# Performance work log

Measured on AMD Instinct MI355X. Metric: run time of the kernel, lower is better.

The kernel has to match this reference:

```python
import jax, jax.numpy as jnp
import numpy as np

DEPTH = 4
SCALE = 1.0


def _exp_levels(v, depth):
    # Tensor-algebra exponential of a linear segment with increment v: level k = v^{(x)k} / k!
    # v: (B, C); returns tuple of (B, C^k) for k=1..depth
    B = v.shape[0]
    levels = [v]
    for k in range(2, depth + 1):
        levels.append((levels[-1][:, :, None] * v[:, None, :]).reshape(B, -1) / k)
    return tuple(levels)


def _chen_step(levels, v, depth):
    # Chen's identity: S_new = S (x) exp(v), flattened per level.
    e = _exp_levels(v, depth)
    B = v.shape[0]
    new = []
    for k in range(1, depth + 1):
        acc = levels[k - 1] + e[k - 1]
        for i in range(1, k):
            acc = acc + (levels[i - 1][:, :, None] * e[k - i - 1][:, None, :]).reshape(B, -1)
        new.append(acc)
    return tuple(new)


def signature(path, depth):
    # path: (B, T, C) -> concatenated signature levels (B, C + C^2 + ... + C^depth)
    dx = path[:, 1:] - path[:, :-1]          # (B, T-1, C)
    init = _exp_levels(dx[:, 0], depth)      # signature of first segment
    rest = jnp.moveaxis(dx[:, 1:], 0, 1)     # (T-2, B, C)

    def step(lv, v):
        return _chen_step(lv, v, depth), None

    final, _ = jax.lax.scan(step, init, rest)
    return jnp.concatenate(final, axis=-1)


def setup_inputs() -> dict:
    key = jax.random.key(0)
    k1, k2, k3 = jax.random.split(key, 3)
    N, B, T, C = 4096, 1024, 256, 10
    original = jax.random.normal(k1, (N, T, C), dtype=jnp.float32) * 0.1
    generated = jax.random.normal(k2, (B, T, C), dtype=jnp.float32) * 0.1
    sample_idx = jax.random.permutation(k3, N)[:B].astype(jnp.int64)  # sample without replacement
    return {"original": original, "generated": generated, "sample_idx": sample_idx}


def reference(original, generated, sample_idx):
    sig_orig = signature(original, DEPTH)                  # (N, D)
    selected = sig_orig[sample_idx]                        # (B, D)
    sig_gen = signature(generated, DEPTH)                  # (B, D)
    diff = jnp.mean(selected, axis=0) - jnp.mean(sig_gen, axis=0)
    return jnp.linalg.norm(diff) * SCALE
```

## Files before the change

kernel.cpp:

```cpp
#include <hip/hip_runtime.h>

#define T_LEN 256
#define C_DIM 10
#define NSTEP 255
#define BSZ   1024
#define NBLK  2048
#define D1 10
#define D2 100
#define D3 1000
#define DTOT 11110
#define PATH_ELEMS (T_LEN * C_DIM)
#define DX_ELEMS (NSTEP * C_DIM)
#define DXROW 12

__global__ __launch_bounds__(128, 2) void sig_accum_kernel(
    const float* __restrict__ original,
    const float* __restrict__ generated,
    const int* __restrict__ sample_idx,
    float* __restrict__ ws, int nrep, int store_mode)
{
    const int tid = threadIdx.x;
    const int b   = blockIdx.x;

    __shared__ float s_dx[NSTEP * DXROW];

    const float* path;
    float sign;
    if (b < BSZ) { path = original + (size_t)sample_idx[b] * PATH_ELEMS; sign = 1.0f; }
    else         { path = generated + (size_t)(b - BSZ) * PATH_ELEMS;    sign = -1.0f; }

    for (int idx = tid; idx < DX_ELEMS; idx += 128) {
        int t = idx / C_DIM, c = idx - t * C_DIM;
        s_dx[t * DXROW + c] = path[idx + C_DIM] - path[idx];
    }
    __syncthreads();

    const int m0  = 4 * tid;
    const int k0  = m0 / 100;
    const int ij0 = m0 - k0 * 100;
    const int ia  = ij0 / 10;
    const int ib  = (ij0 + 2) / 10;
    const int j0  = ij0 - ia * 10;
    const int jc  = (j0 + 2) % 10;

    float s1a = 0.0f, s1b = 0.0f;
    float s2[4] = {0.0f, 0.0f, 0.0f, 0.0f};
    float s3[8];
    float acc[8][10];
    #pragma unroll
    for (int r = 0; r < 8; ++r) {
        s3[r] = 0.0f;
        #pragma unroll
        for (int l = 0; l < 10; ++l) acc[r][l] = 0.0f;
    }

    if (tid < 125) {
        const float* vrow = s_dx;
        #pragma unroll 1
        for (int t = 0; t < NSTEP; ++t, vrow += DXROW) {
            const float4 va = *(const float4*)(vrow);
            const float4 vb = *(const float4*)(vrow + 4);
            const float2 vc = *(const float2*)(vrow + 8);
            const float2 vjA = *(const float2*)(vrow + j0);
            const float2 vjB = *(const float2*)(vrow + jc);
            const float via = vrow[ia];
            const float vib = vrow[ib];
            const float vk0 = vrow[k0];
            const float vk1 = vrow[k0 + 5];

            const float vv[10] = {va.x, va.y, va.z, va.w,
                                  vb.x, vb.y, vb.z, vb.w, vc.x, vc.y};
            const float vj[4] = {vjA.x, vjA.y, vjB.x, vjB.y};
            const float vk0h = vk0 * 0.5f;
            const float vk1h = vk1 * 0.5f;

            #pragma unroll
            for (int q = 0; q < 4; ++q) {
                const float s1q = (q < 2) ? s1a : s1b;
                const float viq = (q < 2) ? via : vib;
                const float a2q = s2[q] + (s1q + viq * 0.25f)        * (vj[q] * (1.0f / 3.0f));
                const float b2q = s2[q] + (s1q + viq * (1.0f/3.0f))  * (vj[q] * 0.5f);
                s2[q]           = s2[q] + (s1q + viq * 0.5f)         * vj[q];

                const float a3x = s3[q] + a2q * vk0h;
                s3[q] += b2q * vk0;
                #pragma unroll
                for (int l = 0; l < 10; ++l) acc[q][l] += a3x * vv[l];

                const float a3y = s3[4 + q] + a2q * vk1h;
                s3[4 + q] += b2q * vk1;
                #pragma unroll
                for (int l = 0; l < 10; ++l) acc[4 + q][l] += a3y * vv[l];
            }
            s1a += via;
            s1b += vib;
        }
    }

    if (store_mode) {
        float* orow = ws + (size_t)b * DTOT;
        if (tid < D1) orow[tid] = sign * (path[(T_LEN - 1) * C_DIM + tid] - path[tid]);
        if (tid < 25) {
            #pragma unroll
            for (int q = 0; q < 4; ++q) orow[D1 + ij0 + q] = sign * s2[q];
        }
        if (tid < 125) {
            #pragma unroll
            for (int ch = 0; ch < 2; ++ch) {
                const int kk = k0 + 5 * ch;
                #pragma unroll
                for (int r = 0; r < 4; ++r) {
                    const int idx3 = (ij0 + r) * 10 + kk;
                    orow[D1 + D2 + idx3] = sign * s3[ch * 4 + r];
                    float* p4 = orow + D1 + D2 + D3 + (size_t)idx3 * 10;
                    #pragma unroll
                    for (int l = 0; l < 10; l += 2)
                        *(float2*)&p4[l] = make_float2(sign * acc[ch * 4 + r][l],
                                                       sign * acc[ch * 4 + r][l + 1]);
                }
            }
        }
    } else {
        float* base = ws + (size_t)(b % nrep) * DTOT;
        if (tid < D1)
            atomicAdd(&base[tid], sign * (path[(T_LEN - 1) * C_DIM + tid] - path[tid]));
        if (tid < 25) {
            #pragma unroll
            for (int q = 0; q < 4; ++q) atomicAdd(&base[D1 + ij0 + q], sign * s2[q]);
        }
        if (tid < 125) {
            #pragma unroll
            for (int ch = 0; ch < 2; ++ch) {
                const int kk = k0 + 5 * ch;
                #pragma unroll
                for (int r = 0; r < 4; ++r) {
                    const int idx3 = (ij0 + r) * 10 + kk;
                    atomicAdd(&base[D1 + D2 + idx3], sign * s3[ch * 4 + r]);
                    #pragma unroll
                    for (int l = 0; l < 10; ++l)
                        atomicAdd(&base[D1 + D2 + D3 + idx3 * 10 + l],
                                  sign * acc[ch * 4 + r][l]);
                }
            }
        }
    }
}

__global__ __launch_bounds__(256) void sig_sum_kernel(
    const float* __restrict__ ws, float* __restrict__ accvec)
{
    const int d2 = blockIdx.x * 256 + threadIdx.x;
    if (d2 >= DTOT / 2) return;
    const float* p = ws + (size_t)(blockIdx.y * 32) * DTOT + 2 * d2;
    float sx = 0.0f, sy = 0.0f;
    #pragma unroll
    for (int r = 0; r < 32; ++r) {
        const float2 v = *(const float2*)(p + (size_t)r * DTOT);
        sx += v.x; sy += v.y;
    }
    atomicAdd(&accvec[2 * d2], sx);
    atomicAdd(&accvec[2 * d2 + 1], sy);
}

__global__ __launch_bounds__(256) void sig_sumsq_kernel(
    const float* __restrict__ accvec, float* __restrict__ sumsq,
    unsigned int* __restrict__ counter, float* __restrict__ out, int nblocks)
{
    const int d = blockIdx.x * 256 + threadIdx.x;
    float s = 0.0f;
    if (d < DTOT) { float v = accvec[d]; s = v * v; }
    for (int off = 32; off > 0; off >>= 1) s += __shfl_down(s, off, 64);
    __shared__ float red[4];
    __shared__ unsigned int lastflag;
    if ((threadIdx.x & 63) == 0) red[threadIdx.x >> 6] = s;
    __syncthreads();
    if (threadIdx.x == 0) {
        atomicAdd(sumsq, red[0] + red[1] + red[2] + red[3]);
        __threadfence();
        lastflag = (atomicAdd(counter, 1u) == (unsigned int)(nblocks - 1));
    }
    __syncthreads();
    if (threadIdx.x == 0 && lastflag) {
        __threadfence();
        out[0] = sqrtf(*(volatile float*)sumsq) * (1.0f / (float)BSZ);
    }
}

__global__ __launch_bounds__(256) void sig_reduce_kernel(
    const float* __restrict__ ws, int nrows, float* __restrict__ sumsq,
    unsigned int* __restrict__ counter, float* __restrict__ out, int nblocks)
{
    const int d = blockIdx.x * 256 + threadIdx.x;
    float s = 0.0f;
    if (d < DTOT) {
        for (int r = 0; r < nrows; ++r) s += ws[(size_t)r * DTOT + d];
        s = s * s;
    }
    for (int off = 32; off > 0; off >>= 1) s += __shfl_down(s, off, 64);
    __shared__ float red[4];
    __shared__ unsigned int lastflag;
    if ((threadIdx.x & 63) == 0) red[threadIdx.x >> 6] = s;
    __syncthreads();
    if (threadIdx.x == 0) {
        atomicAdd(sumsq, red[0] + red[1] + red[2] + red[3]);
        __threadfence();
        lastflag = (atomicAdd(counter, 1u) == (unsigned int)(nblocks - 1));
    }
    __syncthreads();
    if (threadIdx.x == 0 && lastflag) {
        __threadfence();
        out[0] = sqrtf(*(volatile float*)sumsq) * (1.0f / (float)BSZ);
    }
}

extern "C" void kernel_launch(void* const* d_in, const int* in_sizes, int n_in,
                              void* d_out, int out_size, void* d_ws, size_t ws_size,
                              hipStream_t stream) {
    const float* original   = (const float*)d_in[0];
    const float* generated  = (const float*)d_in[1];
    const int*   sample_idx = (const int*)d_in[2];
    float* out = (float*)d_out;
    float* ws  = (float*)d_ws;

    const size_t need_store = ((size_t)(NBLK + 1) * DTOT + 2) * sizeof(float);

    if (ws_size >= need_store) {
        float* accvec = ws + (size_t)NBLK * DTOT;
        float* sumsq  = accvec + DTOT;
        unsigned int* counter = (unsigned int*)(sumsq + 1);
        hipMemsetAsync(accvec, 0, (DTOT + 2) * sizeof(float), stream);
        sig_accum_kernel<<<NBLK, 128, 0, stream>>>(original, generated, sample_idx,
                                                   ws, 1, 1);
        dim3 g1((DTOT / 2 + 255) / 256, 64);
        sig_sum_kernel<<<g1, 256, 0, stream>>>(ws, accvec);
        const int nb2 = (DTOT + 255) / 256;
        sig_sumsq_kernel<<<nb2, 256, 0, stream>>>(accvec, sumsq, counter, out, nb2);
    } else {
        int nrep = 1;
        if (ws_size >= ((size_t)64 * DTOT + 2) * sizeof(float)) nrep = 64;
        else if (ws_size >= ((size_t)8 * DTOT + 2) * sizeof(float)) nrep = 8;
        float* sumsq = ws + (size_t)nrep * DTOT;
        unsigned int* counter = (unsigned int*)(sumsq + 1);
        hipMemsetAsync(ws, 0, ((size_t)nrep * DTOT + 2) * sizeof(float), stream);
        sig_accum_kernel<<<NBLK, 128, 0, stream>>>(original, generated, sample_idx,
                                                   ws, nrep, 0);
        const int nb2 = (DTOT + 255) / 256;
        sig_reduce_kernel<<<nb2, 256, 0, stream>>>(ws, nrep, sumsq, counter, out, nb2);
    }
}
```

Baseline: 304.5 us.

## Pair original and generated paths per block with finer per-thread work split

Each block now processes one original/generated pair in two sequential passes and keeps the signed difference in registers, so it writes one signature row per pair instead of two. Threads go from 125 active of 128 to 500 active of 512, each owning two level-3 entries instead of eight. This cuts registers per thread, raises occupancy, and halves both workspace writes and the downstream sum work. In exchange each block runs the serial time loop twice with a shared-memory refill and extra barriers between passes.

```diff
diff --git a/kernel.cpp b/kernel.cpp
--- a/kernel.cpp
+++ b/kernel.cpp
@@ -4,7 +4,7 @@
 #define C_DIM 10
 #define NSTEP 255
 #define BSZ   1024
-#define NBLK  2048
+#define NPAIR 1024
 #define D1 10
 #define D2 100
 #define D3 1000
@@ -13,7 +13,7 @@
 #define DX_ELEMS (NSTEP * C_DIM)
 #define DXROW 12
 
-__global__ __launch_bounds__(128, 2) void sig_accum_kernel(
+__global__ __launch_bounds__(512, 8) void sig_accum_kernel(
     const float* __restrict__ original,
     const float* __restrict__ generated,
     const int* __restrict__ sample_idx,
@@ -24,123 +24,120 @@
 
     __shared__ float s_dx[NSTEP * DXROW];
 
-    const float* path;
-    float sign;
-    if (b < BSZ) { path = original + (size_t)sample_idx[b] * PATH_ELEMS; sign = 1.0f; }
-    else         { path = generated + (size_t)(b - BSZ) * PATH_ELEMS;    sign = -1.0f; }
-
-    for (int idx = tid; idx < DX_ELEMS; idx += 128) {
-        int t = idx / C_DIM, c = idx - t * C_DIM;
-        s_dx[t * DXROW + c] = path[idx + C_DIM] - path[idx];
-    }
-    __syncthreads();
-
-    const int m0  = 4 * tid;
-    const int k0  = m0 / 100;
-    const int ij0 = m0 - k0 * 100;
+    const float* path_gen  = generated + (size_t)b * PATH_ELEMS;
+    const float* path_orig = original + (size_t)sample_idx[b] * PATH_ELEMS;
+
+    const int m0  = 2 * tid;
+    const int k   = m0 / 100;
+    const int ij0 = m0 - k * 100;
     const int ia  = ij0 / 10;
-    const int ib  = (ij0 + 2) / 10;
     const int j0  = ij0 - ia * 10;
-    const int jc  = (j0 + 2) % 10;
-
-    float s1a = 0.0f, s1b = 0.0f;
-    float s2[4] = {0.0f, 0.0f, 0.0f, 0.0f};
-    float s3[8];
-    float acc[8][10];
+
+    float s1a = 0.0f;
+    float s2[2]  = {0.0f, 0.0f};
+    float s3[2]  = {0.0f, 0.0f};
+    float s2o[2] = {0.0f, 0.0f};
+    float s3o[2] = {0.0f, 0.0f};
+    float acc[2][10];
     #pragma unroll
-    for (int r = 0; r < 8; ++r) {
-        s3[r] = 0.0f;
+    for (int q = 0; q < 2; ++q)
         #pragma unroll
-        for (int l = 0; l < 10; ++l) acc[r][l] = 0.0f;
-    }
-
-    if (tid < 125) {
-        const float* vrow = s_dx;
-        #pragma unroll 1
-        for (int t = 0; t < NSTEP; ++t, vrow += DXROW) {
-            const float4 va = *(const float4*)(vrow);
-            const float4 vb = *(const float4*)(vrow + 4);
-            const float2 vc = *(const float2*)(vrow + 8);
-            const float2 vjA = *(const float2*)(vrow + j0);
-            const float2 vjB = *(const float2*)(vrow + jc);
-            const float via = vrow[ia];
-            const float vib = vrow[ib];
-            const float vk0 = vrow[k0];
-            const float vk1 = vrow[k0 + 5];
-
-            const float vv[10] = {va.x, va.y, va.z, va.w,
-                                  vb.x, vb.y, vb.z, vb.w, vc.x, vc.y};
-            const float vj[4] = {vjA.x, vjA.y, vjB.x, vjB.y};
-            const float vk0h = vk0 * 0.5f;
-            const float vk1h = vk1 * 0.5f;
-
+        for (int l = 0; l < 10; ++l) acc[q][l] = 0.0f;
+
+    #pragma unroll 1
+    for (int pass = 0; pass < 2; ++pass) {
+        const float* path = (pass == 0) ? path_gen : path_orig;
+
+        for (int idx = tid; idx < DX_ELEMS; idx += 512) {
+            int t = idx / C_DIM, c = idx - t * C_DIM;
+            s_dx[t * DXROW + c] = path[idx + C_DIM] - path[idx];
+        }
+        __syncthreads();
+
+        if (tid < 500) {
+            const float* vrow = s_dx;
+            #pragma unroll 1
+            for (int t = 0; t < NSTEP; ++t, vrow += DXROW) {
+                const float4 va = *(const float4*)(vrow);
+                const float4 vb = *(const float4*)(vrow + 4);
+                const float2 vc = *(const float2*)(vrow + 8);
+                const float2 vjp = *(const float2*)(vrow + j0);
+                const float via = vrow[ia];
+                const float vk  = vrow[k];
+
+                const float vv[10] = {va.x, va.y, va.z, va.w,
+                                      vb.x, vb.y, vb.z, vb.w, vc.x, vc.y};
+                const float vj[2] = {vjp.x, vjp.y};
+                const float vkh = vk * 0.5f;
+                const float t1 = s1a + via * 0.25f;
+                const float t2 = s1a + via * (1.0f / 3.0f);
+                const float t3 = s1a + via * 0.5f;
+
+                #pragma unroll
+                for (int q = 0; q < 2; ++q) {
+                    const float a2 = s2[q] + t1 * (vj[q] * (1.0f / 3.0f));
+                    const float b2 = s2[q] + t2 * (vj[q] * 0.5f);
+                    s2[q]          = s2[q] + t3 * vj[q];
+                    const float a3 = s3[q] + a2 * vkh;
+                    s3[q] += b2 * vk;
+                    #pragma unroll
+                    for (int l = 0; l < 10; ++l) acc[q][l] += a3 * vv[l];
+                }
+                s1a += via;
+            }
+        }
+
+        if (pass == 0) {
             #pragma unroll
-            for (int q = 0; q < 4; ++q) {
-                const float s1q = (q < 2) ? s1a : s1b;
-                const float viq = (q < 2) ? via : vib;
-                const float a2q = s2[q] + (s1q + viq * 0.25f)        * (vj[q] * (1.0f / 3.0f));
-                const float b2q = s2[q] + (s1q + viq * (1.0f/3.0f))  * (vj[q] * 0.5f);
-                s2[q]           = s2[q] + (s1q + viq * 0.5f)         * vj[q];
-
-                const float a3x = s3[q] + a2q * vk0h;
-                s3[q] += b2q * vk0;
-                #pragma unroll
-                for (int l = 0; l < 10; ++l) acc[q][l] += a3x * vv[l];
-
-                const float a3y = s3[4 + q] + a2q * vk1h;
-                s3[4 + q] += b2q * vk1;
-                #pragma unroll
-                for (int l = 0; l < 10; ++l) acc[4 + q][l] += a3y * vv[l];
-            }
-            s1a += via;
-            s1b += vib;
+            for (int q = 0; q < 2; ++q) {
+                s2o[q] = -s2[q];  s2[q] = 0.0f;
+                s3o[q] = -s3[q];  s3[q] = 0.0f;
+                #pragma unroll
+                for (int l = 0; l < 10; ++l) acc[q][l] = -acc[q][l];
+            }
+            s1a = 0.0f;
+            __syncthreads();
         }
     }
 
     if (store_mode) {
-        float* orow = ws + (size_t)b * DTOT;
-        if (tid < D1) orow[tid] = sign * (path[(T_LEN - 1) * C_DIM + tid] - path[tid]);
-        if (tid < 25) {
+        float* row = ws + (size_t)b * DTOT;
+        if (tid < D1)
+            row[tid] = (path_orig[(T_LEN - 1) * C_DIM + tid] - path_orig[tid])
+                     - (path_gen[(T_LEN - 1) * C_DIM + tid] - path_gen[tid]);
+        if (tid < 50) {
+            row[D1 + ij0]     = s2o[0] + s2[0];
+            row[D1 + ij0 + 1] = s2o[1] + s2[1];
+        }
+        if (tid < 500) {
             #pragma unroll
-            for (int q = 0; q < 4; ++q) orow[D1 + ij0 + q] = sign * s2[q];
-        }
-        if (tid < 125) {
-            #pragma unroll
-            for (int ch = 0; ch < 2; ++ch) {
-                const int kk = k0 + 5 * ch;
-                #pragma unroll
-                for (int r = 0; r < 4; ++r) {
-                    const int idx3 = (ij0 + r) * 10 + kk;
-                    orow[D1 + D2 + idx3] = sign * s3[ch * 4 + r];
-                    float* p4 = orow + D1 + D2 + D3 + (size_t)idx3 * 10;
-                    #pragma unroll
-                    for (int l = 0; l < 10; l += 2)
-                        *(float2*)&p4[l] = make_float2(sign * acc[ch * 4 + r][l],
-                                                       sign * acc[ch * 4 + r][l + 1]);
-                }
+            for (int q = 0; q < 2; ++q) {
+                const int idx3 = (ij0 + q) * 10 + k;
+                row[D1 + D2 + idx3] = s3o[q] + s3[q];
+                float* p4 = row + D1 + D2 + D3 + (size_t)idx3 * 10;
+                #pragma unroll
+                for (int l = 0; l < 10; l += 2)
+                    *(float2*)&p4[l] = make_float2(acc[q][l], acc[q][l + 1]);
             }
         }
     } else {
         float* base = ws + (size_t)(b % nrep) * DTOT;
         if (tid < D1)
-            atomicAdd(&base[tid], sign * (path[(T_LEN - 1) * C_DIM + tid] - path[tid]));
-        if (tid < 25) {
+            atomicAdd(&base[tid],
+                      (path_orig[(T_LEN - 1) * C_DIM + tid] - path_orig[tid])
+                    - (path_gen[(T_LEN - 1) * C_DIM + tid] - path_gen[tid]));
+        if (tid < 50) {
+            atomicAdd(&base[D1 + ij0],     s2o[0] + s2[0]);
+            atomicAdd(&base[D1 + ij0 + 1], s2o[1] + s2[1]);
+        }
+        if (tid < 500) {
             #pragma unroll
-            for (int q = 0; q < 4; ++q) atomicAdd(&base[D1 + ij0 + q], sign * s2[q]);
-        }
-        if (tid < 125) {
-            #pragma unroll
-            for (int ch = 0; ch < 2; ++ch) {
-                const int kk = k0 + 5 * ch;
-                #pragma unroll
-                for (int r = 0; r < 4; ++r) {
-                    const int idx3 = (ij0 + r) * 10 + kk;
-                    atomicAdd(&base[D1 + D2 + idx3], sign * s3[ch * 4 + r]);
-                    #pragma unroll
-                    for (int l = 0; l < 10; ++l)
-                        atomicAdd(&base[D1 + D2 + D3 + idx3 * 10 + l],
-                                  sign * acc[ch * 4 + r][l]);
-                }
+            for (int q = 0; q < 2; ++q) {
+                const int idx3 = (ij0 + q) * 10 + k;
+                atomicAdd(&base[D1 + D2 + idx3], s3o[q] + s3[q]);
+                #pragma unroll
+                for (int l = 0; l < 10; ++l)
+                    atomicAdd(&base[D1 + D2 + D3 + idx3 * 10 + l], acc[q][l]);
             }
         }
     }
@@ -222,16 +219,16 @@
     float* out = (float*)d_out;
     float* ws  = (float*)d_ws;
 
-    const size_t need_store = ((size_t)(NBLK + 1) * DTOT + 2) * sizeof(float);
+    const size_t need_store = ((size_t)(NPAIR + 1) * DTOT + 2) * sizeof(float);
 
     if (ws_size >= need_store) {
-        float* accvec = ws + (size_t)NBLK * DTOT;
+        float* accvec = ws + (size_t)NPAIR * DTOT;
         float* sumsq  = accvec + DTOT;
         unsigned int* counter = (unsigned int*)(sumsq + 1);
         hipMemsetAsync(accvec, 0, (DTOT + 2) * sizeof(float), stream);
-        sig_accum_kernel<<<NBLK, 128, 0, stream>>>(original, generated, sample_idx,
-                                                   ws, 1, 1);
-        dim3 g1((DTOT / 2 + 255) / 256, 64);
+        sig_accum_kernel<<<NPAIR, 512, 0, stream>>>(original, generated, sample_idx,
+                                                    ws, 1, 1);
+        dim3 g1((DTOT / 2 + 255) / 256, 32);
         sig_sum_kernel<<<g1, 256, 0, stream>>>(ws, accvec);
         const int nb2 = (DTOT + 255) / 256;
         sig_sumsq_kernel<<<nb2, 256, 0, stream>>>(accvec, sumsq, counter, out, nb2);
@@ -242,8 +239,8 @@
         float* sumsq = ws + (size_t)nrep * DTOT;
         unsigned int* counter = (unsigned int*)(sumsq + 1);
         hipMemsetAsync(ws, 0, ((size_t)nrep * DTOT + 2) * sizeof(float), stream);
-        sig_accum_kernel<<<NBLK, 128, 0, stream>>>(original, generated, sample_idx,
-                                                   ws, nrep, 0);
+        sig_accum_kernel<<<NPAIR, 512, 0, stream>>>(original, generated, sample_idx,
+                                                    ws, nrep, 0);
         const int nb2 = (DTOT + 255) / 256;
         sig_reduce_kernel<<<nb2, 256, 0, stream>>>(ws, nrep, sumsq, counter, out, nb2);
     }
```

After: 345.3 us. 13.4% more time.
